# Kernel tuning notes

Measured on AMD Instinct MI355X. Metric: run time of the kernel, lower is better.

The kernel has to match this reference:

```python
import jax, jax.numpy as jnp
import numpy as np

B, T, F = 256, 512, 64      # batch, input_win, feature_m
U1, U2, OUT = 256, 128, 24  # GRU1 units, GRU2 units, output_win


def _gru_seq(x, K, R, b):
    """Keras GRU (reset_after=True, tanh/sigmoid). x: [B,T,F] -> [B,T,U].
    K: [F,3U] input kernel, R: [U,3U] recurrent kernel, b: [2,3U] (input bias, recurrent bias).
    Gate order: z (update), r (reset), h (candidate).
    """
    u = R.shape[0]
    # Precompute all input projections in one big GEMM: [B,T,3U]
    xg = jnp.einsum('btf,fg->btg', x, K) + b[0]

    def step(h, xt):
        rg = h @ R + b[1]                       # [B,3U] recurrent projection
        xz, xr, xh = jnp.split(xt, 3, axis=-1)
        rz, rr, rh = jnp.split(rg, 3, axis=-1)
        z = jax.nn.sigmoid(xz + rz)
        r = jax.nn.sigmoid(xr + rr)
        hh = jnp.tanh(xh + r * rh)              # reset_after: r applied after matmul
        hn = z * h + (1.0 - z) * hh
        return hn, hn

    h0 = jnp.zeros((x.shape[0], u), x.dtype)
    _, hs = jax.lax.scan(step, h0, jnp.swapaxes(xg, 0, 1))  # scan over time
    return jnp.swapaxes(hs, 0, 1)  # [B,T,U]


def setup_inputs() -> dict:
    key = jax.random.key(0)
    ks = jax.random.split(key, 12)
    s = lambda k, shape: jax.random.normal(k, shape, jnp.float32) * 0.05
    return {
        'x':  jax.random.normal(ks[0], (B, T, F), jnp.float32),
        'k1': s(ks[1], (F, 3 * U1)),
        'r1': s(ks[2], (U1, 3 * U1)),
        'b1': jnp.zeros((2, 3 * U1), jnp.float32),
        'k2': s(ks[3], (U1, 3 * U2)),
        'r2': s(ks[4], (U2, 3 * U2)),
        'b2': jnp.zeros((2, 3 * U2), jnp.float32),
        'w3': s(ks[5], (U2, 64)),  'b3': jnp.zeros((64,), jnp.float32),
        'w4': s(ks[6], (64, 32)),  'b4': jnp.zeros((32,), jnp.float32),
        'w5': s(ks[7], (32, OUT)), 'b5': jnp.zeros((OUT,), jnp.float32),
    }


def reference(x, k1, r1, b1, k2, r2, b2, w3, b3, w4, b4, w5, b5):
    h = _gru_seq(x, k1, r1, b1)            # [B,T,256]
    h = _gru_seq(h, k2, r2, b2)[:, -1]     # return_sequences=False -> last state [B,128]
    h = h @ w3 + b3                        # Dense(64), linear activation
    h = h @ w4 + b4                        # Dense(32)
    return h @ w5 + b5                     # Dense(output_win)
```

## Files before the change

kernel.cpp:

```cpp
#include <hip/hip_runtime.h>
#include <hip/hip_fp16.h>
#include <math.h>

#define BATCH 256
#define TSEQ  512
#define FEAT  64
#define NU1   256
#define NU2   128

#define G1Z_OFF 0
#define G1R_OFF 40960
#define G1H_OFF 81920
#define G2Z_OFF 122880
#define G2R_OFF 147456
#define G2H_OFF 172032
#define TOTAL_H2 196608

#define G1Z_U4 0
#define G1R_U4 10240
#define G1H_U4 20480
#define G2Z_U4 30720
#define G2R_U4 36864
#define G2H_U4 43008

#define LDS_PARK_BYTES (9216 * 16)

typedef _Float16 h2f __attribute__((ext_vector_type(2)));

__device__ __forceinline__ float sigmoid_f(float v) {
    return 1.0f / (1.0f + __expf(-v));
}
__device__ __forceinline__ float tanh_f(float v) {
    float c = fminf(fmaxf(v, -15.0f), 15.0f);
    float e = __expf(2.0f * c);
    return (e - 1.0f) / (e + 1.0f);
}

__device__ __forceinline__ h2f bch2(unsigned int u) {
    return __builtin_bit_cast(h2f, u);
}
__device__ __forceinline__ unsigned int pack2(float a, float b) {
    h2f v;
    v.x = (_Float16)a;
    v.y = (_Float16)b;
    return __builtin_bit_cast(unsigned int, v);
}

__device__ __forceinline__ void dot4(float& acc, uint4 w, uint4 a) {
    acc = __builtin_amdgcn_fdot2(bch2(w.x), bch2(a.x), acc, false);
    acc = __builtin_amdgcn_fdot2(bch2(w.y), bch2(a.y), acc, false);
    acc = __builtin_amdgcn_fdot2(bch2(w.z), bch2(a.z), acc, false);
    acc = __builtin_amdgcn_fdot2(bch2(w.w), bch2(a.w), acc, false);
}

__global__ void pack_weights(const float* __restrict__ k1, const float* __restrict__ r1,
                             const float* __restrict__ k2, const float* __restrict__ r2,
                             __half2* __restrict__ ws)
{
    int idx = blockIdx.x * 256 + threadIdx.x;
    if (idx >= TOTAL_H2) return;
    float a, b;
    if (idx < G2Z_OFF) {
        int plane = idx / 40960;
        int rem   = idx % 40960;
        int cc    = rem >> 10;
        int col   = (rem >> 2) & 255;
        int q     = rem & 3;
        int kh    = cc / 20;
        int c     = cc - kh * 20;
        int g     = plane * 256 + col;
        int pair  = (c < 4) ? ((kh * 4 + c) * 4 + q)
                            : (32 + (kh * 16 + (c - 4)) * 4 + q);
        int row0  = pair * 2;
        if (row0 < 64) { a = k1[row0 * 768 + g];        b = k1[(row0 + 1) * 768 + g]; }
        else           { a = r1[(row0 - 64) * 768 + g]; b = r1[(row0 - 63) * 768 + g]; }
    } else {
        int idx2  = idx - G2Z_OFF;
        int plane = idx2 / 24576;
        int rem   = idx2 % 24576;
        int cc    = rem >> 9;
        int col   = (rem >> 2) & 127;
        int q     = rem & 3;
        int kq    = cc / 12;
        int c     = cc - kq * 12;
        int g     = plane * 128 + col;
        int pair  = (c < 8) ? ((kq * 8 + c) * 4 + q)
                            : (128 + (kq * 4 + (c - 8)) * 4 + q);
        int row0  = pair * 2;
        if (row0 < 256) { a = k2[row0 * 384 + g];         b = k2[(row0 + 1) * 384 + g]; }
        else            { a = r2[(row0 - 256) * 384 + g]; b = r2[(row0 - 255) * 384 + g]; }
    }
    __half2 h;
    h.x = __float2half_rn(a);
    h.y = __float2half_rn(b);
    ws[idx] = h;
}

template <int COLS, int NCH>
__device__ __forceinline__ void seg3p(const uint4* __restrict__ pz,
                                      const uint4* __restrict__ pr,
                                      const uint4* __restrict__ ph,
                                      const unsigned int* __restrict__ act,
                                      float& az, float& ar, float& a3)
{
    static_assert(NCH % 4 == 0, "NCH must be a multiple of 4");
    uint4 a_z0 = pz[0], a_z1 = pz[COLS];
    uint4 a_r0 = pr[0], a_r1 = pr[COLS];
    uint4 a_h0 = ph[0], a_h1 = ph[COLS];
    uint4 va0 = *(const uint4*)(act);
    uint4 va1 = *(const uint4*)(act + 4);
    #pragma unroll 1
    for (int c = 0; c < NCH; c += 4) {
        const uint4* qz = pz + 2 * COLS;
        const uint4* qr = pr + 2 * COLS;
        const uint4* qh = ph + 2 * COLS;
        uint4 b_z0 = qz[0], b_z1 = qz[COLS];
        uint4 b_r0 = qr[0], b_r1 = qr[COLS];
        uint4 b_h0 = qh[0], b_h1 = qh[COLS];
        const uint4 vb0 = *(const uint4*)(act + 8);
        const uint4 vb1 = *(const uint4*)(act + 12);
        dot4(az, a_z0, va0); dot4(ar, a_r0, va0); dot4(a3, a_h0, va0);
        dot4(az, a_z1, va1); dot4(ar, a_r1, va1); dot4(a3, a_h1, va1);
        pz += 4 * COLS; pr += 4 * COLS; ph += 4 * COLS;
        act += 16;
        if (c + 4 < NCH) {
            a_z0 = pz[0]; a_z1 = pz[COLS];
            a_r0 = pr[0]; a_r1 = pr[COLS];
            a_h0 = ph[0]; a_h1 = ph[COLS];
            va0 = *(const uint4*)(act);
            va1 = *(const uint4*)(act + 4);
        }
        dot4(az, b_z0, vb0); dot4(ar, b_r0, vb0); dot4(a3, b_h0, vb0);
        dot4(az, b_z1, vb1); dot4(ar, b_r1, vb1); dot4(a3, b_h1, vb1);
    }
}

template <int COLS>
__device__ __forceinline__ void seg_pair(const uint4* __restrict__ pz,
                                         const uint4* __restrict__ pr,
                                         const uint4* __restrict__ ph,
                                         const unsigned int* __restrict__ act,
                                         float& az, float& ar, float& a3)
{
    const uint4 v0 = *(const uint4*)(act);
    const uint4 v1 = *(const uint4*)(act + 4);
    uint4 z0 = pz[0], z1 = pz[COLS];
    uint4 r0 = pr[0], r1 = pr[COLS];
    uint4 h0 = ph[0], h1 = ph[COLS];
    dot4(az, z0, v0); dot4(ar, r0, v0); dot4(a3, h0, v0);
    dot4(az, z1, v1); dot4(ar, r1, v1); dot4(a3, h1, v1);
}

__global__ __launch_bounds__(512, 2)
void gru_fused(const float* __restrict__ x,
               const float* __restrict__ b1, const float* __restrict__ b2,
               const float* __restrict__ w3, const float* __restrict__ b3,
               const float* __restrict__ w4, const float* __restrict__ b4,
               const float* __restrict__ w5, const float* __restrict__ b5,
               const unsigned int* __restrict__ wp,
               float* __restrict__ out)
{
    extern __shared__ __align__(16) uint4 lwdyn[];
    uint4* lw2 = lwdyn;
    uint4* lw1 = lwdyn + 6144;
    __shared__ __align__(16) unsigned int act1[2][160];
    __shared__ __align__(16) unsigned int act2[2][64];
    __shared__ __align__(16) unsigned int act1s[2][160];
    __shared__ float h2fin[NU2];
    __shared__ float d3[64];
    __shared__ float d4[32];

    const int tid = threadIdx.x;
    const int row = blockIdx.x;
    const int j   = tid >> 1;
    const int kh  = tid & 1;
    const int c2  = tid >> 2;
    const int kq  = tid & 3;

    const uint4* wp4 = (const uint4*)wp;

    for (int i = tid; i < 6144; i += 512) {
        int cg = i >> 9;
        int c  = cg / 3, g = cg - 3 * c;
        lw2[i] = wp4[G2Z_U4 + g * 6144 + (kq * 12 + 8 + c) * 128 + c2];
    }
    for (int i = tid; i < 3072; i += 512) {
        int cg = i >> 9;
        int c  = cg / 3, g = cg - 3 * c;
        lw1[i] = wp4[G1Z_U4 + g * 10240 + (kh * 20 + c) * 256 + j];
    }

    for (int i = tid; i < 2 * 160; i += 512) (&act1[0][0])[i]  = 0u;
    for (int i = tid; i < 2 * 64;  i += 512) (&act2[0][0])[i]  = 0u;
    for (int i = tid; i < 2 * 160; i += 512) (&act1s[0][0])[i] = 0u;

    const float bm1  = (kh == 0) ? 1.0f : 0.0f;
    const float bz1  = (b1[j] + b1[768 + j]) * bm1;
    const float br1  = (b1[256 + j] + b1[1024 + j]) * bm1;
    const float bxh1 = b1[512 + j] * bm1;
    const float brh1 = b1[1280 + j] * bm1;
    const float bm2  = (kq == 0) ? 1.0f : 0.0f;
    const float bz2  = (b2[c2] + b2[384 + c2]) * bm2;
    const float br2  = (b2[128 + c2] + b2[512 + c2]) * bm2;
    const float bxh2 = b2[256 + c2] * bm2;
    const float brh2 = b2[640 + c2] * bm2;

    const uint4* g1z = wp4 + G1Z_U4 + (kh * 20) * 256 + j;
    const uint4* g1r = wp4 + G1R_U4 + (kh * 20) * 256 + j;
    const uint4* g1h = wp4 + G1H_U4 + (kh * 20) * 256 + j;
    const uint4* g2z = wp4 + G2Z_U4 + (kq * 12) * 128 + c2;
    const uint4* g2r = wp4 + G2R_U4 + (kq * 12) * 128 + c2;
    const uint4* g2h = wp4 + G2H_U4 + (kq * 12) * 128 + c2;
    const uint4* l2 = lw2 + tid;
    const uint4* l1 = lw1 + tid;

    __syncthreads();

    if (tid < FEAT) {
        float x0 = x[(size_t)row * TSEQ * FEAT + tid];
        float xb = __shfl_xor(x0, 1);
        if ((tid & 1) == 0) act1[0][tid >> 1] = pack2(x0, xb);
    }
    __syncthreads();

    float hp1 = 0.0f;
    float hp2 = 0.0f;

    for (int t = 0; t < TSEQ; ++t) {
        const int cur = t & 1, nb = cur ^ 1;

        float xpre = 0.0f;
        if (t + 1 < TSEQ && tid < FEAT)
            xpre = x[(size_t)row * TSEQ * FEAT + (t + 1) * FEAT + tid];

        float az = bz1, ar = br1, aA = bxh1, aB = brh1;
        seg_pair<1536>(l1, l1 + 512, l1 + 1024,
                       &act1[cur][kh * 16], az, ar, aA);
        seg_pair<256>(g1z + 2 * 256, g1r + 2 * 256, g1h + 2 * 256,
                      &act1[cur][kh * 16 + 8], az, ar, aA);
        seg3p<256, 16>(g1z + 4 * 256, g1r + 4 * 256, g1h + 4 * 256,
                       &act1[cur][32 + kh * 64], az, ar, aB);
        az += __shfl_xor(az, 1);
        ar += __shfl_xor(ar, 1);
        aA += __shfl_xor(aA, 1);
        aB += __shfl_xor(aB, 1);
        {
            const float z  = sigmoid_f(az);
            const float rg = sigmoid_f(ar);
            const float hh = tanh_f(aA + rg * aB);
            const float hn = z * hp1 + (1.0f - z) * hh;
            hp1 = hn;
            const float hnb = __shfl_xor(hn, 2);
            if ((tid & 3) == 0) {
                const unsigned int pk = pack2(hn, hnb);
                const int p = tid >> 2;
                act1[nb][32 + p] = pk;
                act1s[nb][(p >> 5) * 40 + (p & 31)] = pk;
            }
        }
        if (t + 1 < TSEQ && tid < FEAT) {
            float xb = __shfl_xor(xpre, 1);
            if ((tid & 1) == 0) act1[nb][tid >> 1] = pack2(xpre, xb);
        }
        __syncthreads();

        float az2 = bz2, ar2 = br2, aA2 = bxh2, aB2 = brh2;
        seg3p<128, 8>(g2z, g2r, g2h, &act1s[nb][kq * 40], az2, ar2, aA2);
        seg3p<1536, 4>(l2, l2 + 512, l2 + 1024,
                       &act2[cur][kq * 16], az2, ar2, aB2);
        az2 += __shfl_xor(az2, 1); az2 += __shfl_xor(az2, 2);
        ar2 += __shfl_xor(ar2, 1); ar2 += __shfl_xor(ar2, 2);
        aA2 += __shfl_xor(aA2, 1); aA2 += __shfl_xor(aA2, 2);
        aB2 += __shfl_xor(aB2, 1); aB2 += __shfl_xor(aB2, 2);
        {
            const float z2v = sigmoid_f(az2);
            const float rg2 = sigmoid_f(ar2);
            const float hh2 = tanh_f(aA2 + rg2 * aB2);
            const float hn2 = z2v * hp2 + (1.0f - z2v) * hh2;
            hp2 = hn2;
            const float hnb2 = __shfl_xor(hn2, 4);
            if ((tid & 7) == 0) act2[nb][tid >> 3] = pack2(hn2, hnb2);
        }
    }

    if ((tid & 3) == 0) h2fin[c2] = hp2;
    __syncthreads();

    if (tid < 64) {
        float a = b3[tid];
        #pragma unroll 4
        for (int u = 0; u < NU2; ++u) a += h2fin[u] * w3[u * 64 + tid];
        d3[tid] = a;
    }
    __syncthreads();
    if (tid < 32) {
        float a = b4[tid];
        #pragma unroll 4
        for (int u = 0; u < 64; ++u) a += d3[u] * w4[u * 32 + tid];
        d4[tid] = a;
    }
    __syncthreads();
    if (tid < 24) {
        float a = b5[tid];
        #pragma unroll 4
        for (int u = 0; u < 32; ++u) a += d4[u] * w5[u * 24 + tid];
        out[(size_t)row * 24 + tid] = a;
    }
}

extern "C" void kernel_launch(void* const* d_in, const int* in_sizes, int n_in,
                              void* d_out, int out_size, void* d_ws, size_t ws_size,
                              hipStream_t stream) {
    (void)in_sizes; (void)n_in; (void)ws_size; (void)out_size;
    const float* x  = (const float*)d_in[0];
    const float* k1 = (const float*)d_in[1];
    const float* r1 = (const float*)d_in[2];
    const float* b1 = (const float*)d_in[3];
    const float* k2 = (const float*)d_in[4];
    const float* r2 = (const float*)d_in[5];
    const float* b2 = (const float*)d_in[6];
    const float* w3 = (const float*)d_in[7];
    const float* b3 = (const float*)d_in[8];
    const float* w4 = (const float*)d_in[9];
    const float* b4 = (const float*)d_in[10];
    const float* w5 = (const float*)d_in[11];
    const float* b5 = (const float*)d_in[12];
    float* out = (float*)d_out;

    static bool lds_attr_set = false;
    if (!lds_attr_set) {
        (void)hipFuncSetAttribute((const void*)gru_fused,
                                  hipFuncAttributeMaxDynamicSharedMemorySize,
                                  LDS_PARK_BYTES);
        lds_attr_set = true;
    }

    hipLaunchKernelGGL(pack_weights, dim3((TOTAL_H2 + 255) / 256), dim3(256), 0, stream,
                       k1, r1, k2, r2, (__half2*)d_ws);
    hipLaunchKernelGGL(gru_fused, dim3(BATCH), dim3(512), LDS_PARK_BYTES, stream,
                       x, b1, b2, w3, b3, w4, b4, w5, b5,
                       (const unsigned int*)d_ws, out);
}
```

Before: 4.742 ms.

## Quantize GRU1 recurrent weights to FP8 with per-column scales

```diff
diff --git a/kernel.cpp b/kernel.cpp
--- a/kernel.cpp
+++ b/kernel.cpp
@@ -7,14 +7,6 @@
 #define FEAT  64
 #define NU1   256
 #define NU2   128
-
-#define G1Z_OFF 0
-#define G1R_OFF 40960
-#define G1H_OFF 81920
-#define G2Z_OFF 122880
-#define G2R_OFF 147456
-#define G2H_OFF 172032
-#define TOTAL_H2 196608
 
 #define G1Z_U4 0
 #define G1R_U4 10240
@@ -22,10 +14,14 @@
 #define G2Z_U4 30720
 #define G2R_U4 36864
 #define G2H_U4 43008
+#define TOTAL_H2 196608
+
+#define FP8_SC_BYTE 49152
 
 #define LDS_PARK_BYTES (9216 * 16)
 
 typedef _Float16 h2f __attribute__((ext_vector_type(2)));
+typedef float f32x2 __attribute__((ext_vector_type(2)));
 
 __device__ __forceinline__ float sigmoid_f(float v) {
     return 1.0f / (1.0f + __expf(-v));
@@ -35,22 +31,75 @@
     float e = __expf(2.0f * c);
     return (e - 1.0f) / (e + 1.0f);
 }
-
 __device__ __forceinline__ h2f bch2(unsigned int u) {
     return __builtin_bit_cast(h2f, u);
 }
 __device__ __forceinline__ unsigned int pack2(float a, float b) {
-    h2f v;
-    v.x = (_Float16)a;
-    v.y = (_Float16)b;
+    h2f v; v.x = (_Float16)a; v.y = (_Float16)b;
     return __builtin_bit_cast(unsigned int, v);
 }
-
 __device__ __forceinline__ void dot4(float& acc, uint4 w, uint4 a) {
     acc = __builtin_amdgcn_fdot2(bch2(w.x), bch2(a.x), acc, false);
     acc = __builtin_amdgcn_fdot2(bch2(w.y), bch2(a.y), acc, false);
     acc = __builtin_amdgcn_fdot2(bch2(w.z), bch2(a.z), acc, false);
     acc = __builtin_amdgcn_fdot2(bch2(w.w), bch2(a.w), acc, false);
+}
+
+#if __has_builtin(__builtin_amdgcn_cvt_pk_f32_fp8)
+__device__ __forceinline__ f32x2 cvtpk8_lo(unsigned int u) {
+    return __builtin_amdgcn_cvt_pk_f32_fp8((int)u, false);
+}
+__device__ __forceinline__ f32x2 cvtpk8_hi(unsigned int u) {
+    return __builtin_amdgcn_cvt_pk_f32_fp8((int)u, true);
+}
+#else
+__device__ __forceinline__ float fp8dec1(unsigned int b) {
+    float m = __uint_as_float((b & 0x7fu) << 20) * 0x1p+120f;
+    return (b & 0x80u) ? -m : m;
+}
+__device__ __forceinline__ f32x2 cvtpk8_lo(unsigned int u) {
+    f32x2 r; r.x = fp8dec1(u & 0xffu); r.y = fp8dec1((u >> 8) & 0xffu);
+    return r;
+}
+__device__ __forceinline__ f32x2 cvtpk8_hi(unsigned int u) {
+    f32x2 r; r.x = fp8dec1((u >> 16) & 0xffu); r.y = fp8dec1((u >> 24) & 0xffu);
+    return r;
+}
+#endif
+
+__device__ __forceinline__ void dot16f8(float& acc, uint4 w,
+                                        float4 a0, float4 a1, float4 a2, float4 a3) {
+    f32x2 l, h;
+    l = cvtpk8_lo(w.x); h = cvtpk8_hi(w.x);
+    acc = fmaf(l.x, a0.x, acc); acc = fmaf(l.y, a0.y, acc);
+    acc = fmaf(h.x, a0.z, acc); acc = fmaf(h.y, a0.w, acc);
+    l = cvtpk8_lo(w.y); h = cvtpk8_hi(w.y);
+    acc = fmaf(l.x, a1.x, acc); acc = fmaf(l.y, a1.y, acc);
+    acc = fmaf(h.x, a1.z, acc); acc = fmaf(h.y, a1.w, acc);
+    l = cvtpk8_lo(w.z); h = cvtpk8_hi(w.z);
+    acc = fmaf(l.x, a2.x, acc); acc = fmaf(l.y, a2.y, acc);
+    acc = fmaf(h.x, a2.z, acc); acc = fmaf(h.y, a2.w, acc);
+    l = cvtpk8_lo(w.w); h = cvtpk8_hi(w.w);
+    acc = fmaf(l.x, a3.x, acc); acc = fmaf(l.y, a3.y, acc);
+    acc = fmaf(h.x, a3.z, acc); acc = fmaf(h.y, a3.w, acc);
+}
+
+__device__ unsigned char enc_e4m3(float v) {
+    float a = fabsf(v);
+    if (!(a > 0.0f)) return 0;
+    unsigned s = (__float_as_uint(v) >> 31) ? 0x80u : 0u;
+    a = fminf(a, 448.0f);
+    int e; float m = frexpf(a, &e);
+    int E = e - 1; float sig = 2.0f * m;
+    if (E < -6) {
+        float q = rintf(a * 512.0f);
+        if (q >= 8.0f) return (unsigned char)(s | 0x08u);
+        return (unsigned char)(s | (unsigned)q);
+    }
+    float f = rintf((sig - 1.0f) * 8.0f);
+    if (f >= 8.0f) { E += 1; f = 0.0f; }
+    if (E > 8) return (unsigned char)(s | 0x7Eu);
+    return (unsigned char)(s | ((unsigned)(E + 7) << 3) | (unsigned)f);
 }
 
 __global__ void pack_weights(const float* __restrict__ k1, const float* __restrict__ r1,
@@ -60,7 +109,7 @@
     int idx = blockIdx.x * 256 + threadIdx.x;
     if (idx >= TOTAL_H2) return;
     float a, b;
-    if (idx < G2Z_OFF) {
+    if (idx < 122880) {
         int plane = idx / 40960;
         int rem   = idx % 40960;
         int cc    = rem >> 10;
@@ -75,7 +124,7 @@
         if (row0 < 64) { a = k1[row0 * 768 + g];        b = k1[(row0 + 1) * 768 + g]; }
         else           { a = r1[(row0 - 64) * 768 + g]; b = r1[(row0 - 63) * 768 + g]; }
     } else {
-        int idx2  = idx - G2Z_OFF;
+        int idx2  = idx - 122880;
         int plane = idx2 / 24576;
         int rem   = idx2 % 24576;
         int cc    = rem >> 9;
@@ -94,6 +143,24 @@
     h.x = __float2half_rn(a);
     h.y = __float2half_rn(b);
     ws[idx] = h;
+}
+
+__global__ void pack_fp8(const float* __restrict__ r1, char* __restrict__ wsb)
+{
+    int g   = blockIdx.x;
+    int col = threadIdx.x;
+    float mx = 0.0f;
+    for (int r = 0; r < 256; ++r)
+        mx = fmaxf(mx, fabsf(r1[r * 768 + g * 256 + col]));
+    float s = fmaxf(mx * (1.0f / 448.0f), 1e-30f);
+    ((float*)(wsb + FP8_SC_BYTE))[g * 256 + col] = s;
+    float inv = 1.0f / s;
+    for (int r = 0; r < 256; ++r) {
+        float w = r1[r * 768 + g * 256 + col] * inv;
+        int kh = r >> 7, f = (r >> 4) & 7, b = r & 15;
+        wsb[(size_t)(g * 10240 + kh * 5120 + 1024 + f * 256 + col) * 16 + b] =
+            (char)enc_e4m3(w);
+    }
 }
 
 template <int COLS, int NCH>
@@ -151,6 +218,7 @@
     dot4(az, z1, v1); dot4(ar, r1, v1); dot4(a3, h1, v1);
 }
 
+template <bool FP8>
 __global__ __launch_bounds__(512, 2)
 void gru_fused(const float* __restrict__ x,
                const float* __restrict__ b1, const float* __restrict__ b2,
@@ -166,6 +234,7 @@
     __shared__ __align__(16) unsigned int act1[2][160];
     __shared__ __align__(16) unsigned int act2[2][64];
     __shared__ __align__(16) unsigned int act1s[2][160];
+    __shared__ __align__(16) float act1f[2][256];
     __shared__ float h2fin[NU2];
     __shared__ float d3[64];
     __shared__ float d4[32];
@@ -178,6 +247,7 @@
     const int kq  = tid & 3;
 
     const uint4* wp4 = (const uint4*)wp;
+    const char*  wpb = (const char*)wp;
 
     for (int i = tid; i < 6144; i += 512) {
         int cg = i >> 9;
@@ -189,10 +259,10 @@
         int c  = cg / 3, g = cg - 3 * c;
         lw1[i] = wp4[G1Z_U4 + g * 10240 + (kh * 20 + c) * 256 + j];
     }
-
     for (int i = tid; i < 2 * 160; i += 512) (&act1[0][0])[i]  = 0u;
     for (int i = tid; i < 2 * 64;  i += 512) (&act2[0][0])[i]  = 0u;
     for (int i = tid; i < 2 * 160; i += 512) (&act1s[0][0])[i] = 0u;
+    for (int i = tid; i < 2 * 256; i += 512) (&act1f[0][0])[i] = 0.0f;
 
     const float bm1  = (kh == 0) ? 1.0f : 0.0f;
     const float bz1  = (b1[j] + b1[768 + j]) * bm1;
@@ -214,6 +284,13 @@
     const uint4* l2 = lw2 + tid;
     const uint4* l1 = lw1 + tid;
 
+    const uint4* q8zb = wp4 + kh * 5120 + 1024 + j;
+    float s_z = 0.0f, s_r = 0.0f, s_h = 0.0f;
+    if constexpr (FP8) {
+        const float* sc = (const float*)(wpb + FP8_SC_BYTE);
+        s_z = sc[j]; s_r = sc[256 + j]; s_h = sc[512 + j];
+    }
+
     __syncthreads();
 
     if (tid < FEAT) {
@@ -238,8 +315,70 @@
                        &act1[cur][kh * 16], az, ar, aA);
         seg_pair<256>(g1z + 2 * 256, g1r + 2 * 256, g1h + 2 * 256,
                       &act1[cur][kh * 16 + 8], az, ar, aA);
-        seg3p<256, 16>(g1z + 4 * 256, g1r + 4 * 256, g1h + 4 * 256,
-                       &act1[cur][32 + kh * 64], az, ar, aB);
+        if constexpr (FP8) {
+            float z8 = 0.0f, r8 = 0.0f, h8 = 0.0f;
+            const float* af = &act1f[cur][kh * 128];
+            const uint4* qz = q8zb;
+            uint4 a_z0 = qz[0], a_z1 = qz[256];
+            uint4 a_r0 = qz[10240], a_r1 = qz[10240 + 256];
+            uint4 a_h0 = qz[20480], a_h1 = qz[20480 + 256];
+            #pragma unroll 1
+            for (int f = 0; f < 8; f += 4) {
+                const uint4* bz = qz + 2 * 256;
+                uint4 b_z0 = bz[0], b_z1 = bz[256];
+                uint4 b_r0 = bz[10240], b_r1 = bz[10240 + 256];
+                uint4 b_h0 = bz[20480], b_h1 = bz[20480 + 256];
+                {
+                    const float4 a0 = *(const float4*)(af);
+                    const float4 a1 = *(const float4*)(af + 4);
+                    const float4 a2 = *(const float4*)(af + 8);
+                    const float4 a3 = *(const float4*)(af + 12);
+                    dot16f8(z8, a_z0, a0, a1, a2, a3);
+                    dot16f8(r8, a_r0, a0, a1, a2, a3);
+                    dot16f8(h8, a_h0, a0, a1, a2, a3);
+                }
+                {
+                    const float4 a0 = *(const float4*)(af + 16);
+                    const float4 a1 = *(const float4*)(af + 20);
+                    const float4 a2 = *(const float4*)(af + 24);
+                    const float4 a3 = *(const float4*)(af + 28);
+                    dot16f8(z8, a_z1, a0, a1, a2, a3);
+                    dot16f8(r8, a_r1, a0, a1, a2, a3);
+                    dot16f8(h8, a_h1, a0, a1, a2, a3);
+                }
+                qz += 4 * 256;
+                if (f + 4 < 8) {
+                    a_z0 = qz[0]; a_z1 = qz[256];
+                    a_r0 = qz[10240]; a_r1 = qz[10240 + 256];
+                    a_h0 = qz[20480]; a_h1 = qz[20480 + 256];
+                }
+                {
+                    const float4 a0 = *(const float4*)(af + 32);
+                    const float4 a1 = *(const float4*)(af + 36);
+                    const float4 a2 = *(const float4*)(af + 40);
+                    const float4 a3 = *(const float4*)(af + 44);
+                    dot16f8(z8, b_z0, a0, a1, a2, a3);
+                    dot16f8(r8, b_r0, a0, a1, a2, a3);
+                    dot16f8(h8, b_h0, a0, a1, a2, a3);
+                }
+                {
+                    const float4 a0 = *(const float4*)(af + 48);
+                    const float4 a1 = *(const float4*)(af + 52);
+                    const float4 a2 = *(const float4*)(af + 56);
+                    const float4 a3 = *(const float4*)(af + 60);
+                    dot16f8(z8, b_z1, a0, a1, a2, a3);
+                    dot16f8(r8, b_r1, a0, a1, a2, a3);
+                    dot16f8(h8, b_h1, a0, a1, a2, a3);
+                }
+                af += 64;
+            }
+            az = fmaf(s_z, z8, az);
+            ar = fmaf(s_r, r8, ar);
+            aB = fmaf(s_h, h8, aB);
+        } else {
+            seg3p<256, 16>(g1z + 4 * 256, g1r + 4 * 256, g1h + 4 * 256,
+                           &act1[cur][32 + kh * 64], az, ar, aB);
+        }
         az += __shfl_xor(az, 1);
         ar += __shfl_xor(ar, 1);
         aA += __shfl_xor(aA, 1);
@@ -250,6 +389,9 @@
             const float hh = tanh_f(aA + rg * aB);
             const float hn = z * hp1 + (1.0f - z) * hh;
             hp1 = hn;
+            if constexpr (FP8) {
+                if (kh == 0) act1f[nb][j] = hn;
+            }
             const float hnb = __shfl_xor(hn, 2);
             if ((tid & 3) == 0) {
                 const unsigned int pk = pack2(hn, hnb);
@@ -311,7 +453,7 @@
 extern "C" void kernel_launch(void* const* d_in, const int* in_sizes, int n_in,
                               void* d_out, int out_size, void* d_ws, size_t ws_size,
                               hipStream_t stream) {
-    (void)in_sizes; (void)n_in; (void)ws_size; (void)out_size;
+    (void)in_sizes; (void)n_in; (void)out_size; (void)ws_size;
     const float* x  = (const float*)d_in[0];
     const float* k1 = (const float*)d_in[1];
     const float* r1 = (const float*)d_in[2];
@@ -329,7 +471,10 @@
 
     static bool lds_attr_set = false;
     if (!lds_attr_set) {
-        (void)hipFuncSetAttribute((const void*)gru_fused,
+        (void)hipFuncSetAttribute((const void*)gru_fused<true>,
+                                  hipFuncAttributeMaxDynamicSharedMemorySize,
+                                  LDS_PARK_BYTES);
+        (void)hipFuncSetAttribute((const void*)gru_fused<false>,
                                   hipFuncAttributeMaxDynamicSharedMemorySize,
                                   LDS_PARK_BYTES);
         lds_attr_set = true;
@@ -337,7 +482,9 @@
 
     hipLaunchKernelGGL(pack_weights, dim3((TOTAL_H2 + 255) / 256), dim3(256), 0, stream,
                        k1, r1, k2, r2, (__half2*)d_ws);
-    hipLaunchKernelGGL(gru_fused, dim3(BATCH), dim3(512), LDS_PARK_BYTES, stream,
-                       x, b1, b2, w3, b3, w4, b4, w5, b5,
+    hipLaunchKernelGGL(pack_fp8, dim3(3), dim3(256), 0, stream,
+                       r1, (char*)d_ws);
+    hipLaunchKernelGGL((gru_fused<true>), dim3(BATCH), dim3(512), LDS_PARK_BYTES,
+                       stream, x, b1, b2, w3, b3, w4, b4, w5, b5,
                        (const unsigned int*)d_ws, out);
 }
```

Measured after the change: 4.050 ms. 1.17x faster.
